# Optimization experiments

Measured on AMD Instinct MI355X. Metric: run time of the kernel, lower is better.

## Reference

```python
import jax, jax.numpy as jnp
import numpy as np

N = 50000      # nodes
E = 800000     # edges (before self loops)
D_IN = 64      # input atom feature dim
HID = 128      # hidden_dim
HEADS = 4
C = HID // HEADS  # 32 per-head channels
ED = 12        # edge feature dim
L = 4          # num GAT layers
EPS = 1e-5


def setup_inputs() -> dict:
    key = jax.random.key(0)
    ks = jax.random.split(key, 10)
    s = 0.1
    return {
        "x": jax.random.normal(ks[0], (N, D_IN), jnp.float32),
        "edge_index": jax.random.randint(ks[1], (2, E), 0, N, dtype=jnp.int32),
        "edge_attr": jax.random.uniform(ks[2], (E, ED), jnp.float32),
        "Wp": jax.random.normal(ks[3], (D_IN, HID), jnp.float32) * s,
        "bp": jnp.zeros((HID,), jnp.float32),
        "W": jax.random.normal(ks[4], (L, HID, HID), jnp.float32) * s,
        "We": jax.random.normal(ks[5], (L, ED, HID), jnp.float32) * s,
        "att_src": jax.random.normal(ks[6], (L, HEADS, C), jnp.float32) * s,
        "att_dst": jax.random.normal(ks[7], (L, HEADS, C), jnp.float32) * s,
        "att_edge": jax.random.normal(ks[8], (L, HEADS, C), jnp.float32) * s,
        "bias": jnp.zeros((L, HID), jnp.float32),
        "gamma": jnp.ones((L, HID), jnp.float32),
        "beta": jnp.zeros((L, HID), jnp.float32),
    }


def _gat_layer(h, src, dst, ea_full, W, We, a_s, a_d, a_e, b):
    # PyG GATConv: x' = x W -> [N, heads, C]; attention uses edge features, msg = alpha * x'_src
    xp = (h @ W).reshape(N, HEADS, C)
    e_emb = (ea_full @ We).reshape(-1, HEADS, C)          # [E', heads, C]
    a_src = (xp * a_s).sum(-1)                            # [N, heads]
    a_dst = (xp * a_d).sum(-1)
    a = a_src[src] + a_dst[dst] + (e_emb * a_e).sum(-1)   # [E', heads]
    a = jax.nn.leaky_relu(a, 0.2)
    # segment softmax over destination node neighborhoods
    amax = jax.ops.segment_max(a, dst, num_segments=N)
    ex = jnp.exp(a - amax[dst])
    denom = jax.ops.segment_sum(ex, dst, num_segments=N)
    alpha = ex / denom[dst]                               # [E', heads]
    msg = alpha[:, :, None] * xp[src]                     # [E', heads, C]
    out = jax.ops.segment_sum(msg, dst, num_segments=N)   # [N, heads, C]
    return out.reshape(N, HID) + b


def reference(x, edge_index, edge_attr, Wp, bp, W, We, att_src, att_dst, att_edge, bias, gamma, beta):
    # PyG GATConv add_self_loops=True with fill_value='mean' for edge_attr
    loop = jnp.arange(N, dtype=edge_index.dtype)
    src = jnp.concatenate([edge_index[0], loop])
    dst = jnp.concatenate([edge_index[1], loop])
    ea_mean = edge_attr.mean(0)
    ea_full = jnp.concatenate([edge_attr, jnp.broadcast_to(ea_mean, (N, ED))], 0)

    h = jax.nn.relu(x @ Wp + bp)
    for i in range(L):
        h_in = h
        h = _gat_layer(h, src, dst, ea_full, W[i], We[i], att_src[i], att_dst[i], att_edge[i], bias[i])
        # BatchNorm1d (training-mode batch statistics)
        mu = h.mean(0)
        var = ((h - mu) ** 2).mean(0)
        h = gamma[i] * (h - mu) / jnp.sqrt(var + EPS) + beta[i]
        h = jax.nn.relu(h)
        if i > 0:
            h = h + h_in
    return h
```

## Files before the change

kernel.cpp:

```cpp
#include <hip/hip_runtime.h>

constexpr int N_NODES = 50000;
constexpr int N_EDGES = 800000;
constexpr int N_ETOT  = N_EDGES + N_NODES;
constexpr int HID     = 128;
constexpr int HEADS   = 4;
constexpr int ED      = 12;
constexpr int LAYERS  = 4;
constexpr float BN_EPS = 1e-5f;
constexpr int EB = (N_ETOT + 255) / 256;
constexpr int GB = (N_NODES + 63) / 64;
constexpr int WB = (LAYERS * HID * HID + 255) / 256;
constexpr int CHUNK  = 2048;
constexpr int NCHUNK = (N_ETOT + CHUNK - 1) / CHUNK;
constexpr int NB     = (N_NODES + 127) / 128;
constexpr int F_TOT  = NB * NCHUNK;
constexpr int SB3    = (F_TOT + 255) / 256;

typedef __attribute__((ext_vector_type(8))) short short8;
typedef __attribute__((ext_vector_type(4))) float floatx4;

__device__ inline unsigned bf16pair(float a, float b) {
    unsigned ua = __float_as_uint(a), ub = __float_as_uint(b);
    ua = (ua + 0x7FFFu + ((ua >> 16) & 1u)) >> 16;
    ub = (ub + 0x7FFFu + ((ub >> 16) & 1u)) >> 16;
    return ua | (ub << 16);
}

__launch_bounds__(256)
__global__ void pre1_kernel(const int* __restrict__ dst, int* __restrict__ counts,
                            const float* __restrict__ ea, float* __restrict__ easum,
                            const float* __restrict__ W, unsigned short* __restrict__ wb,
                            const float* __restrict__ A, const float* __restrict__ B,
                            const float* __restrict__ bias, float* __restrict__ C,
                            unsigned* __restrict__ Cb) {
    __shared__ float smem[64 * 128];
    int bid = blockIdx.x, t = threadIdx.x;
    if (bid < GB) {
        constexpr int K = 64;
        const float4* B4 = (const float4*)B;
        float4* Bs4 = (float4*)smem;
#pragma unroll
        for (int i = t; i < K * 32; i += 256) Bs4[i] = B4[i];
        __syncthreads();

        int c0 = (t & 15) * 8;
        int r0 = (t >> 4) * 4;
        int rbase = bid * 64 + r0;

        float acc[4][8];
#pragma unroll
        for (int j = 0; j < 4; j++)
#pragma unroll
            for (int c = 0; c < 8; c++) acc[j][c] = 0.f;

        const float4* A4 = (const float4*)A;
        int rg[4];
#pragma unroll
        for (int j = 0; j < 4; j++) rg[j] = min(rbase + j, N_NODES - 1);

        for (int kk = 0; kk < K; kk += 4) {
            float4 av[4];
#pragma unroll
            for (int j = 0; j < 4; j++) av[j] = A4[(size_t)rg[j] * (K / 4) + (kk >> 2)];
            float a_arr[4][4];
#pragma unroll
            for (int j = 0; j < 4; j++) {
                a_arr[j][0] = av[j].x; a_arr[j][1] = av[j].y;
                a_arr[j][2] = av[j].z; a_arr[j][3] = av[j].w;
            }
#pragma unroll
            for (int jj = 0; jj < 4; jj++) {
                float4 b0 = Bs4[(kk + jj) * 32 + (c0 >> 2)];
                float4 b1 = Bs4[(kk + jj) * 32 + (c0 >> 2) + 1];
#pragma unroll
                for (int j = 0; j < 4; j++) {
                    float a = a_arr[j][jj];
                    acc[j][0] += a * b0.x; acc[j][1] += a * b0.y;
                    acc[j][2] += a * b0.z; acc[j][3] += a * b0.w;
                    acc[j][4] += a * b1.x; acc[j][5] += a * b1.y;
                    acc[j][6] += a * b1.z; acc[j][7] += a * b1.w;
                }
            }
        }

#pragma unroll
        for (int j = 0; j < 4; j++) {
            int r = rbase + j;
            if (r < N_NODES) {
                float o[8];
#pragma unroll
                for (int c = 0; c < 8; c++) o[c] = fmaxf(acc[j][c] + bias[c0 + c], 0.f);
                ((float4*)(C + (size_t)r * 128 + c0))[0] = make_float4(o[0], o[1], o[2], o[3]);
                ((float4*)(C + (size_t)r * 128 + c0 + 4))[0] = make_float4(o[4], o[5], o[6], o[7]);
                uint4 pk;
                pk.x = bf16pair(o[0], o[1]); pk.y = bf16pair(o[2], o[3]);
                pk.z = bf16pair(o[4], o[5]); pk.w = bf16pair(o[6], o[7]);
                ((uint4*)(Cb + (size_t)r * 64 + (c0 >> 1)))[0] = pk;
            }
        }
    } else if (bid < GB + NCHUNK) {
        int chunk = bid - GB;
        int* lh = (int*)smem;
        for (int i = t; i < NB; i += 256) lh[i] = 0;
        __syncthreads();
        int e0 = chunk * CHUNK;
        int eend = min(e0 + CHUNK, N_ETOT);
        for (int e = e0 + t; e < eend; e += 256) {
            int d = (e < N_EDGES) ? dst[e] : (e - N_EDGES);
            atomicAdd(&lh[d >> 7], 1);
        }
        __syncthreads();
        for (int i = t; i < NB; i += 256) counts[(size_t)chunk * NB + i] = lh[i];
    } else if (bid < GB + NCHUNK + 256) {
        int b2 = bid - GB - NCHUNK;
        float* ls = smem;
        if (t < 12) ls[t] = 0.f;
        __syncthreads();
        float loc[12];
#pragma unroll
        for (int d = 0; d < 12; d++) loc[d] = 0.f;
        for (int e = b2 * 256 + t; e < N_EDGES; e += 256 * 256) {
            const float* er = ea + (size_t)e * ED;
#pragma unroll
            for (int d = 0; d < 12; d++) loc[d] += er[d];
        }
#pragma unroll
        for (int d = 0; d < 12; d++) atomicAdd(&ls[d], loc[d]);
        __syncthreads();
        if (t < 12) atomicAdd(&easum[t], ls[t]);
    } else {
        int idx = (bid - GB - NCHUNK - 256) * 256 + t;
        if (idx < LAYERS * HID * HID) {
            int l = idx >> 14;
            int k = (idx >> 7) & 127;
            int n = idx & 127;
            unsigned u = __float_as_uint(W[idx]);
            u = (u + 0x7FFFu + ((u >> 16) & 1u)) >> 16;
            int kt = k >> 5, q = (k & 31) >> 3, j = k & 7;
            int nt = n >> 4, c = n & 15;
            int lane = q * 16 + c;
            wb[(size_t)l * 16384 + ((size_t)(kt * 8 + nt) * 64 + lane) * 8 + j] =
                (unsigned short)u;
        }
    }
}

__global__ void blocksum2_kernel(const int* __restrict__ counts, int* __restrict__ bsum) {
    __shared__ int sd[256];
    int t = threadIdx.x;
    int j = blockIdx.x * 256 + t;
    int v = 0;
    if (j < F_TOT) {
        int bb = j / NCHUNK, cc = j - bb * NCHUNK;
        v = counts[(size_t)cc * NB + bb];
    }
    sd[t] = v;
    __syncthreads();
#pragma unroll
    for (int off = 128; off; off >>= 1) {
        if (t < off) sd[t] += sd[t + off];
        __syncthreads();
    }
    if (t == 0) bsum[blockIdx.x] = sd[0];
}

__launch_bounds__(256)
__global__ void pre2_kernel(const int* __restrict__ bsum, int* __restrict__ boff,
                            int* __restrict__ chunkbase, int* __restrict__ rowp,
                            const float* __restrict__ easum,
                            const float* __restrict__ We, const float* __restrict__ att_edge,
                            float* __restrict__ wea_all, float* __restrict__ aloop) {
    int t = threadIdx.x;
    if (blockIdx.x == 0) {
        __shared__ int sd[256];
        int b = 3 * t;
        int v0 = (b + 0 < SB3) ? bsum[b + 0] : 0;
        int v1 = (b + 1 < SB3) ? bsum[b + 1] : 0;
        int v2 = (b + 2 < SB3) ? bsum[b + 2] : 0;
        int tot = v0 + v1 + v2;
        sd[t] = tot;
        __syncthreads();
#pragma unroll
        for (int off = 1; off < 256; off <<= 1) {
            int u = (t >= off) ? sd[t - off] : 0;
            __syncthreads();
            sd[t] += u;
            __syncthreads();
        }
        int excl = sd[t] - tot;
        if (b + 0 < SB3) boff[b + 0] = excl;
        if (b + 1 < SB3) boff[b + 1] = excl + v0;
        if (b + 2 < SB3) boff[b + 2] = excl + v0 + v1;
        if (t == 255) {
            chunkbase[F_TOT] = sd[255];
            rowp[N_NODES] = N_ETOT;
        }
    } else {
        __shared__ float em[12];
        __shared__ float weash[LAYERS * ED * HEADS];
        if (t < 12) em[t] = easum[t] / (float)N_EDGES;
        if (t < LAYERS * ED * HEADS) {
            int l = t / (ED * HEADS);
            int r = t % (ED * HEADS);
            int d = r / HEADS;
            int h = r % HEADS;
            float sum = 0.f;
#pragma unroll
            for (int c = 0; c < 32; c++)
                sum += We[((size_t)(l * ED + d)) * HID + h * 32 + c] *
                       att_edge[(l * HEADS + h) * 32 + c];
            wea_all[t] = sum;
            weash[t] = sum;
        }
        __syncthreads();
        if (t < LAYERS * HEADS) {
            int l = t / HEADS, h = t % HEADS;
            float s = 0.f;
#pragma unroll
            for (int d = 0; d < 12; d++) s += em[d] * weash[l * ED * HEADS + d * HEADS + h];
            aloop[t] = s;
        }
    }
}

__global__ void addback_kernel(const int* __restrict__ counts, const int* __restrict__ boff,
                               int* __restrict__ chunkbase) {
    __shared__ int sd[256];
    int t = threadIdx.x;
    int j = blockIdx.x * 256 + t;
    int v = 0;
    if (j < F_TOT) {
        int bb = j / NCHUNK, cc = j - bb * NCHUNK;
        v = counts[(size_t)cc * NB + bb];
    }
    sd[t] = v;
    __syncthreads();
#pragma unroll
    for (int off = 1; off < 256; off <<= 1) {
        int u = (t >= off) ? sd[t - off] : 0;
        __syncthreads();
        sd[t] += u;
        __syncthreads();
    }
    if (j < F_TOT) chunkbase[j] = sd[t] - v + boff[blockIdx.x];
}

__launch_bounds__(256)
__global__ void pre3_kernel(const unsigned short* __restrict__ hAb,
                            const unsigned short* __restrict__ wb,
                            const float* __restrict__ att_s, const float* __restrict__ att_d,
                            unsigned* __restrict__ xpb,
                            float* __restrict__ asrc, float* __restrict__ adst,
                            const int* __restrict__ src, const int* __restrict__ dst,
                            const int* __restrict__ chunkbase, int2* __restrict__ bucketed) {
    __shared__ float smem[4 * 16 * 129];
    int t = threadIdx.x;
    if (blockIdx.x >= GB) {
        int chunk = blockIdx.x - GB;
        int* lb = (int*)smem;
        int* lh = lb + NB;
        for (int i = t; i < NB; i += 256) {
            lb[i] = chunkbase[(size_t)i * NCHUNK + chunk];
            lh[i] = 0;
        }
        __syncthreads();
        int e0 = chunk * CHUNK;
        int eend = min(e0 + CHUNK, N_ETOT);
        for (int e = e0 + t; e < eend; e += 256) {
            int s, d;
            if (e < N_EDGES) { s = src[e]; d = dst[e]; }
            else             { s = d = e - N_EDGES; }
            int b = d >> 7;
            int lr = atomicAdd(&lh[b], 1);
            bucketed[lb[b] + lr] = make_int2(s, e | ((d & 127) << 20));
        }
        return;
    }
    int bid = blockIdx.x;
    float (*lds)[16][129] = (float (*)[16][129])smem;
    int w = t >> 6, lane = t & 63;
    int rbase = bid * 64 + w * 16;
    int mrow = lane & 15, quad = lane >> 4;

    floatx4 acc[8];
#pragma unroll
    for (int nt = 0; nt < 8; nt++) acc[nt] = (floatx4){0.f, 0.f, 0.f, 0.f};

    int arow = min(rbase + mrow, N_NODES - 1);
    const short8* wb8 = (const short8*)wb;
#pragma unroll
    for (int kt = 0; kt < 4; kt++) {
        short8 afrag = *(const short8*)(hAb + (size_t)arow * 128 + kt * 32 + quad * 8);
#pragma unroll
        for (int nt = 0; nt < 8; nt++) {
            short8 bfrag = wb8[(kt * 8 + nt) * 64 + lane];
            acc[nt] = __builtin_amdgcn_mfma_f32_16x16x32_bf16(afrag, bfrag, acc[nt], 0, 0, 0);
        }
    }
#pragma unroll
    for (int nt = 0; nt < 8; nt++)
#pragma unroll
        for (int rr = 0; rr < 4; rr++)
            lds[w][quad * 4 + rr][nt * 16 + mrow] = acc[nt][rr];

    int row = lane >> 2, h = lane & 3;
    int r = rbase + row;
    float vals[32];
    float ps = 0.f, pd = 0.f;
#pragma unroll
    for (int c = 0; c < 32; c++) {
        float v = lds[w][row][h * 32 + c];
        vals[c] = v;
        ps += v * att_s[h * 32 + c];
        pd += v * att_d[h * 32 + c];
    }
    if (r < N_NODES) {
        unsigned* dstp = xpb + (size_t)r * 64 + h * 16;
#pragma unroll
        for (int qq = 0; qq < 4; qq++) {
            uint4 o;
            o.x = bf16pair(vals[qq * 8 + 0], vals[qq * 8 + 1]);
            o.y = bf16pair(vals[qq * 8 + 2], vals[qq * 8 + 3]);
            o.z = bf16pair(vals[qq * 8 + 4], vals[qq * 8 + 5]);
            o.w = bf16pair(vals[qq * 8 + 6], vals[qq * 8 + 7]);
            ((uint4*)dstp)[qq] = o;
        }
        asrc[r * 4 + h] = ps;
        adst[r * 4 + h] = pd;
    }
}

__launch_bounds__(256)
__global__ void csrd_kernel(const int2* __restrict__ bucketed, const int* __restrict__ chunkbase,
                            int2* __restrict__ csr, int* __restrict__ rowp) {
    __shared__ int hist[128], exc[128], cur[128];
    int b = blockIdx.x, t = threadIdx.x;
    int base = chunkbase[(size_t)b * NCHUNK];
    int cend = chunkbase[(size_t)(b + 1) * NCHUNK];
    int cnt = cend - base;
    if (t < 128) { hist[t] = 0; cur[t] = 0; }
    __syncthreads();
    for (int i = t; i < cnt; i += 256)
        atomicAdd(&hist[(bucketed[base + i].y >> 20) & 127], 1);
    __syncthreads();
    if (t < 128) exc[t] = hist[t];
    __syncthreads();
#pragma unroll
    for (int off = 1; off < 128; off <<= 1) {
        int u = (t < 128 && t >= off) ? exc[t - off] : 0;
        __syncthreads();
        if (t < 128) exc[t] += u;
        __syncthreads();
    }
    if (t < 128) {
        exc[t] -= hist[t];
        int node = b * 128 + t;
        if (node < N_NODES) rowp[node] = base + exc[t];
    }
    __syncthreads();
    for (int i = t; i < cnt; i += 256) {
        int2 r = bucketed[base + i];
        int dl = (r.y >> 20) & 127;
        int lr = atomicAdd(&cur[dl], 1);
        csr[base + exc[dl] + lr] = make_int2(r.x, r.y & 0xFFFFF);
    }
}

__launch_bounds__(256)
__global__ void pre4_kernel(const int2* __restrict__ csr, const float* __restrict__ ea,
                            const float* __restrict__ wea_all, const float* __restrict__ aloop,
                            uint2* __restrict__ aecsr) {
    __shared__ float wsh[LAYERS * ED * HEADS];
    __shared__ float lsh[LAYERS * HEADS];
    int t = threadIdx.x;
    if (t < LAYERS * ED * HEADS) wsh[t] = wea_all[t];
    if (t < LAYERS * HEADS) lsh[t] = aloop[t];
    __syncthreads();
    int i = blockIdx.x * 256 + t;
    if (i >= N_ETOT) return;
    int e = csr[i].y;
    float a[LAYERS][4];
    if (e < N_EDGES) {
        float er[12];
        const float* ep = ea + (size_t)e * ED;
#pragma unroll
        for (int d = 0; d < 12; d++) er[d] = ep[d];
#pragma unroll
        for (int l = 0; l < LAYERS; l++)
#pragma unroll
            for (int h = 0; h < 4; h++) {
                float s = 0.f;
#pragma unroll
                for (int d = 0; d < 12; d++) s += er[d] * wsh[l * 48 + d * 4 + h];
                a[l][h] = s;
            }
    } else {
#pragma unroll
        for (int l = 0; l < LAYERS; l++)
#pragma unroll
            for (int h = 0; h < 4; h++) a[l][h] = lsh[l * 4 + h];
    }
#pragma unroll
    for (int l = 0; l < LAYERS; l++)
        aecsr[(size_t)l * N_ETOT + i] =
            make_uint2(bf16pair(a[l][0], a[l][1]), bf16pair(a[l][2], a[l][3]));
}

template <int ADD>
__launch_bounds__(256)
__global__ void gemm_fused_kernel(const float* __restrict__ outb,
                                  const float* __restrict__ bnsum,
                                  const float* __restrict__ bnsum2,
                                  const float* __restrict__ gamma,
                                  const float* __restrict__ beta,
                                  float* __restrict__ hA,
                                  const unsigned short* __restrict__ wb,
                                  const float* __restrict__ att_s,
                                  const float* __restrict__ att_d,
                                  unsigned* __restrict__ xpb,
                                  float* __restrict__ asrc, float* __restrict__ adst) {
    __shared__ float lds[4][16][129];
    __shared__ float sc_s[128], sh_s[128];
    int t = threadIdx.x;
    if (t < 128) {
        float mu = bnsum[t] / (float)N_NODES;
        float var = bnsum2[t] / (float)N_NODES - mu * mu;
        float inv = rsqrtf(var + BN_EPS);
        float g = gamma[t] * inv;
        sc_s[t] = g;
        sh_s[t] = beta[t] - mu * g;
    }
    __syncthreads();

    int w = t >> 6, lane = t & 63;
    int rbase = blockIdx.x * 64 + w * 16;
    int mrow = lane & 15, quad = lane >> 4;
    int arow = rbase + mrow;
    bool owner = arow < N_NODES;
    int ar = min(arow, N_NODES - 1);

    floatx4 acc[8];
#pragma unroll
    for (int nt = 0; nt < 8; nt++) acc[nt] = (floatx4){0.f, 0.f, 0.f, 0.f};

    const short8* wb8 = (const short8*)wb;
#pragma unroll
    for (int kt = 0; kt < 4; kt++) {
        int cb = kt * 32 + quad * 8;
        const float4* ob = (const float4*)(outb + (size_t)ar * 128 + cb);
        float4 o0 = ob[0], o1 = ob[1];
        float v[8];
        v[0] = fmaxf(o0.x * sc_s[cb + 0] + sh_s[cb + 0], 0.f);
        v[1] = fmaxf(o0.y * sc_s[cb + 1] + sh_s[cb + 1], 0.f);
        v[2] = fmaxf(o0.z * sc_s[cb + 2] + sh_s[cb + 2], 0.f);
        v[3] = fmaxf(o0.w * sc_s[cb + 3] + sh_s[cb + 3], 0.f);
        v[4] = fmaxf(o1.x * sc_s[cb + 4] + sh_s[cb + 4], 0.f);
        v[5] = fmaxf(o1.y * sc_s[cb + 5] + sh_s[cb + 5], 0.f);
        v[6] = fmaxf(o1.z * sc_s[cb + 6] + sh_s[cb + 6], 0.f);
        v[7] = fmaxf(o1.w * sc_s[cb + 7] + sh_s[cb + 7], 0.f);
        if (ADD) {
            const float4* hp = (const float4*)(hA + (size_t)ar * 128 + cb);
            float4 h0 = hp[0], h1 = hp[1];
            v[0] += h0.x; v[1] += h0.y; v[2] += h0.z; v[3] += h0.w;
            v[4] += h1.x; v[5] += h1.y; v[6] += h1.z; v[7] += h1.w;
        }
        if (owner) {
            float4* hw = (float4*)(hA + (size_t)ar * 128 + cb);
            hw[0] = make_float4(v[0], v[1], v[2], v[3]);
            hw[1] = make_float4(v[4], v[5], v[6], v[7]);
        }
        uint4 pk;
        pk.x = bf16pair(v[0], v[1]); pk.y = bf16pair(v[2], v[3]);
        pk.z = bf16pair(v[4], v[5]); pk.w = bf16pair(v[6], v[7]);
        short8 afrag = *(short8*)&pk;
#pragma unroll
        for (int nt = 0; nt < 8; nt++) {
            short8 bfrag = wb8[(kt * 8 + nt) * 64 + lane];
            acc[nt] = __builtin_amdgcn_mfma_f32_16x16x32_bf16(afrag, bfrag, acc[nt], 0, 0, 0);
        }
    }

#pragma unroll
    for (int nt = 0; nt < 8; nt++)
#pragma unroll
        for (int rr = 0; rr < 4; rr++)
            lds[w][quad * 4 + rr][nt * 16 + mrow] = acc[nt][rr];

    int row = lane >> 2, h = lane & 3;
    int r = rbase + row;
    float vals[32];
    float ps = 0.f, pd = 0.f;
#pragma unroll
    for (int c = 0; c < 32; c++) {
        float v = lds[w][row][h * 32 + c];
        vals[c] = v;
        ps += v * att_s[h * 32 + c];
        pd += v * att_d[h * 32 + c];
    }
    if (r < N_NODES) {
        unsigned* dstp = xpb + (size_t)r * 64 + h * 16;
#pragma unroll
        for (int qq = 0; qq < 4; qq++) {
            uint4 o;
            o.x = bf16pair(vals[qq * 8 + 0], vals[qq * 8 + 1]);
            o.y = bf16pair(vals[qq * 8 + 2], vals[qq * 8 + 3]);
            o.z = bf16pair(vals[qq * 8 + 4], vals[qq * 8 + 5]);
            o.w = bf16pair(vals[qq * 8 + 6], vals[qq * 8 + 7]);
            ((uint4*)dstp)[qq] = o;
        }
        asrc[r * 4 + h] = ps;
        adst[r * 4 + h] = pd;
    }
}

__launch_bounds__(256)
__global__ void node_kernel(const uint2* __restrict__ aecsr, const float* __restrict__ asrc,
                            const float* __restrict__ adst, const int* __restrict__ rowp,
                            const int2* __restrict__ csr, const unsigned* __restrict__ xpb,
                            float* __restrict__ out) {
    int gw = (blockIdx.x * blockDim.x + threadIdx.x) >> 6;
    int lane = threadIdx.x & 63;
    if (gw >= N_NODES) return;
    int sub = lane >> 3;
    int sl  = lane & 7;
    int h   = sl >> 1;
    int beg = rowp[gw], end = rowp[gw + 1];
    const uint4* xp4 = (const uint4*)xpb;
    float adh = adst[gw * 4 + h];

    float a[16];
#pragma unroll
    for (int c = 0; c < 16; c++) a[c] = 0.f;
    float den = 0.f;

#define PROC(JJ)                                                                 \
    {                                                                            \
        int2 se = csr[JJ];                                                       \
        uint2 ae = aecsr[JJ];                                                    \
        unsigned aw = (h & 2) ? ae.y : ae.x;                                     \
        float aeh = __uint_as_float((h & 1) ? (aw & 0xFFFF0000u) : (aw << 16));  \
        float ash = asrc[se.x * 4 + h];                                          \
        uint4 v0 = xp4[(size_t)se.x * 16 + sl * 2];                              \
        uint4 v1 = xp4[(size_t)se.x * 16 + sl * 2 + 1];                          \
        float lg = ash + adh + aeh;                                              \
        lg = (lg > 0.f) ? lg : 0.2f * lg;                                        \
        float ex = __expf(fminf(lg, 60.f));                                      \
        a[0]  += ex * __uint_as_float(v0.x << 16);                               \
        a[1]  += ex * __uint_as_float(v0.x & 0xFFFF0000u);                       \
        a[2]  += ex * __uint_as_float(v0.y << 16);                               \
        a[3]  += ex * __uint_as_float(v0.y & 0xFFFF0000u);                       \
        a[4]  += ex * __uint_as_float(v0.z << 16);                               \
        a[5]  += ex * __uint_as_float(v0.z & 0xFFFF0000u);                       \
        a[6]  += ex * __uint_as_float(v0.w << 16);                               \
        a[7]  += ex * __uint_as_float(v0.w & 0xFFFF0000u);                       \
        a[8]  += ex * __uint_as_float(v1.x << 16);                               \
        a[9]  += ex * __uint_as_float(v1.x & 0xFFFF0000u);                       \
        a[10] += ex * __uint_as_float(v1.y << 16);                               \
        a[11] += ex * __uint_as_float(v1.y & 0xFFFF0000u);                       \
        a[12] += ex * __uint_as_float(v1.z << 16);                               \
        a[13] += ex * __uint_as_float(v1.z & 0xFFFF0000u);                       \
        a[14] += ex * __uint_as_float(v1.w << 16);                               \
        a[15] += ex * __uint_as_float(v1.w & 0xFFFF0000u);                       \
        den += ex;                                                               \
    }

    int j = beg + sub;
    for (; j + 8 < end; j += 16) {
        PROC(j); PROC(j + 8);
    }
    for (; j < end; j += 8) PROC(j);
#undef PROC

#pragma unroll
    for (int c = 0; c < 16; c++) {
        a[c] += __shfl_xor(a[c], 8);
        a[c] += __shfl_xor(a[c], 16);
        a[c] += __shfl_xor(a[c], 32);
    }
    den += __shfl_xor(den, 8);
    den += __shfl_xor(den, 16);
    den += __shfl_xor(den, 32);
    float inv = 1.0f / den;
    if (sub == 0) {
        float* op = out + (size_t)gw * 128 + sl * 16;
        ((float4*)op)[0] = make_float4(a[0] * inv, a[1] * inv, a[2] * inv, a[3] * inv);
        ((float4*)op)[1] = make_float4(a[4] * inv, a[5] * inv, a[6] * inv, a[7] * inv);
        ((float4*)op)[2] = make_float4(a[8] * inv, a[9] * inv, a[10] * inv, a[11] * inv);
        ((float4*)op)[3] = make_float4(a[12] * inv, a[13] * inv, a[14] * inv, a[15] * inv);
    }
}

__launch_bounds__(256)
__global__ void bnstats_kernel(const float* __restrict__ h, float* __restrict__ bnsum,
                               float* __restrict__ bnsum2) {
    __shared__ float ls[256], ls2[256];
    int t = threadIdx.x;
    int c = t & 127, half = t >> 7;
    int r0 = blockIdx.x * 128;
    float s = 0.f, s2 = 0.f;
    int rend = min(r0 + 128, N_NODES);
    for (int r = r0 + half; r < rend; r += 2) {
        float v = h[(size_t)r * 128 + c];
        s += v; s2 += v * v;
    }
    ls[t] = s; ls2[t] = s2;
    __syncthreads();
    if (half == 0) {
        s += ls[t + 128]; s2 += ls2[t + 128];
        atomicAdd(&bnsum[c], s);
        atomicAdd(&bnsum2[c], s2);
    }
}

__launch_bounds__(256)
__global__ void finalupd_kernel(const float* __restrict__ outb, const float* __restrict__ bnsum,
                                const float* __restrict__ bnsum2, const float* __restrict__ gamma,
                                const float* __restrict__ beta, const float* __restrict__ hA,
                                float* __restrict__ dst) {
    __shared__ float sc_s[128], sh_s[128];
    int t = threadIdx.x;
    if (t < 128) {
        float mu = bnsum[t] / (float)N_NODES;
        float var = bnsum2[t] / (float)N_NODES - mu * mu;
        float inv = rsqrtf(var + BN_EPS);
        float g = gamma[t] * inv;
        sc_s[t] = g;
        sh_s[t] = beta[t] - mu * g;
    }
    __syncthreads();
    int i = blockIdx.x * blockDim.x + t;
    if (i >= N_NODES * 32) return;
    int c4 = (i & 31) * 4;
    float4 o = ((const float4*)outb)[i];
    float4 hh = ((const float4*)hA)[i];
    float4 v;
    v.x = fmaxf(o.x * sc_s[c4 + 0] + sh_s[c4 + 0], 0.f) + hh.x;
    v.y = fmaxf(o.y * sc_s[c4 + 1] + sh_s[c4 + 1], 0.f) + hh.y;
    v.z = fmaxf(o.z * sc_s[c4 + 2] + sh_s[c4 + 2], 0.f) + hh.z;
    v.w = fmaxf(o.w * sc_s[c4 + 3] + sh_s[c4 + 3], 0.f) + hh.w;
    ((float4*)dst)[i] = v;
}

extern "C" void kernel_launch(void* const* d_in, const int* in_sizes, int n_in,
                              void* d_out, int out_size, void* d_ws, size_t ws_size,
                              hipStream_t stream) {
    const float* x          = (const float*)d_in[0];
    const int*   edge_index = (const int*)d_in[1];
    const float* edge_attr  = (const float*)d_in[2];
    const float* Wp         = (const float*)d_in[3];
    const float* bp         = (const float*)d_in[4];
    const float* W          = (const float*)d_in[5];
    const float* We         = (const float*)d_in[6];
    const float* att_src    = (const float*)d_in[7];
    const float* att_dst    = (const float*)d_in[8];
    const float* att_edge   = (const float*)d_in[9];
    const float* gamma      = (const float*)d_in[11];
    const float* beta       = (const float*)d_in[12];
    float* outp = (float*)d_out;

    const int* ei_src = edge_index;
    const int* ei_dst = edge_index + N_EDGES;

    char* p = (char*)d_ws;
    auto alloc = [&](size_t nbytes) {
        char* r = p;
        p += (nbytes + 255) & ~(size_t)255;
        return r;
    };
    float* easum    = (float*)alloc(16 * 4);
    float* bnsumall = (float*)alloc((size_t)LAYERS * 256 * 4);
    size_t zero_bytes = (char*)(bnsumall + LAYERS * 256) - (char*)easum;

    float* hA       = (float*)alloc((size_t)N_NODES * 128 * 4);
    unsigned* hAb   = (unsigned*)alloc((size_t)N_NODES * 64 * 4);
    unsigned* xpb   = (unsigned*)alloc((size_t)N_NODES * 64 * 4);
    float* outb     = (float*)alloc((size_t)N_NODES * 128 * 4);
    float* asrc     = (float*)alloc((size_t)N_NODES * 4 * 4);
    float* adst     = (float*)alloc((size_t)N_NODES * 4 * 4);
    float* wea_all  = (float*)alloc((LAYERS * 48 + 16) * 4);
    float* aloop    = wea_all + LAYERS * 48;
    unsigned short* wb = (unsigned short*)alloc((size_t)LAYERS * 16384 * 2);
    int* rowp       = (int*)alloc(((size_t)N_NODES + 1) * 4);
    int* counts     = (int*)alloc((size_t)F_TOT * 4);
    int* chunkbase  = (int*)alloc(((size_t)F_TOT + 1) * 4);
    int2* bucketed  = (int2*)alloc((size_t)N_ETOT * 8);
    int2* csr       = (int2*)alloc((size_t)N_ETOT * 8);
    uint2* aecsr    = (uint2*)alloc((size_t)LAYERS * N_ETOT * 8);
    int* bsum       = (int*)alloc(1024 * 4);
    int* boff       = (int*)alloc(1024 * 4);

    (void)hipMemsetAsync(easum, 0, zero_bytes, stream);

    pre1_kernel<<<GB + NCHUNK + 256 + WB, 256, 0, stream>>>(
        ei_dst, counts, edge_attr, easum, W, wb, x, Wp, bp, hA, hAb);
    blocksum2_kernel<<<SB3, 256, 0, stream>>>(counts, bsum);
    pre2_kernel<<<2, 256, 0, stream>>>(bsum, boff, chunkbase, rowp, easum, We, att_edge,
                                       wea_all, aloop);
    addback_kernel<<<SB3, 256, 0, stream>>>(counts, boff, chunkbase);
    pre3_kernel<<<GB + NCHUNK, 256, 0, stream>>>(
        (const unsigned short*)hAb, wb, att_src, att_dst, xpb, asrc, adst,
        ei_src, ei_dst, chunkbase, bucketed);
    csrd_kernel<<<NB, 256, 0, stream>>>(bucketed, chunkbase, csr, rowp);
    pre4_kernel<<<EB, 256, 0, stream>>>(csr, edge_attr, wea_all, aloop, aecsr);

    for (int l = 0; l < LAYERS; l++) {
        float* bnsum  = bnsumall + l * 256;
        float* bnsum2 = bnsum + 128;
        node_kernel<<<(N_NODES + 3) / 4, 256, 0, stream>>>(
            aecsr + (size_t)l * N_ETOT, asrc, adst, rowp, csr, xpb, outb);
        bnstats_kernel<<<(N_NODES + 127) / 128, 256, 0, stream>>>(outb, bnsum, bnsum2);
        if (l < LAYERS - 1) {
            if (l == 0)
                gemm_fused_kernel<0><<<GB, 256, 0, stream>>>(
                    outb, bnsum, bnsum2, gamma + l * 128, beta + l * 128, hA,
                    wb + (size_t)(l + 1) * 16384, att_src + (l + 1) * 128,
                    att_dst + (l + 1) * 128, xpb, asrc, adst);
            else
                gemm_fused_kernel<1><<<GB, 256, 0, stream>>>(
                    outb, bnsum, bnsum2, gamma + l * 128, beta + l * 128, hA,
                    wb + (size_t)(l + 1) * 16384, att_src + (l + 1) * 128,
                    att_dst + (l + 1) * 128, xpb, asrc, adst);
        } else {
            finalupd_kernel<<<(N_NODES * 32 + 255) / 256, 256, 0, stream>>>(
                outb, bnsum, bnsum2, gamma + l * 128, beta + l * 128, hA, outp);
        }
    }
}
```

Before: 575.2 us.

## Fuse BatchNorm statistics into node aggregation kernel and prefetch GEMM A rows

The separate bnstats pass that re-read the full aggregated output is removed. Each node_kernel block now writes per-block channel sums and sums of squares, built through shared memory, to a partial buffer, and a small bnred kernel reduces these with atomics. The GEMM A-tile loads are also software-prefetched one k-step ahead. This saves a full read of the N×128 output per layer, at the cost of a __syncthreads in node_kernel and an extra partial buffer of NODE_BLKS×256 floats. The early return for out-of-range warps was removed, but N_NODES is divisible by 4, so every warp is valid.

```diff
diff --git a/kernel.cpp b/kernel.cpp
--- a/kernel.cpp
+++ b/kernel.cpp
@@ -11,6 +11,7 @@
 constexpr int EB = (N_ETOT + 255) / 256;
 constexpr int GB = (N_NODES + 63) / 64;
 constexpr int WB = (LAYERS * HID * HID + 255) / 256;
+constexpr int NODE_BLKS = (N_NODES + 3) / 4;
 constexpr int CHUNK  = 2048;
 constexpr int NCHUNK = (N_ETOT + CHUNK - 1) / CHUNK;
 constexpr int NB     = (N_NODES + 127) / 128;
@@ -59,10 +60,16 @@
 #pragma unroll
         for (int j = 0; j < 4; j++) rg[j] = min(rbase + j, N_NODES - 1);
 
+        float4 av[4];
+#pragma unroll
+        for (int j = 0; j < 4; j++) av[j] = A4[(size_t)rg[j] * (K / 4)];
+
         for (int kk = 0; kk < K; kk += 4) {
-            float4 av[4];
-#pragma unroll
-            for (int j = 0; j < 4; j++) av[j] = A4[(size_t)rg[j] * (K / 4) + (kk >> 2)];
+            int kn = (kk + 4 < K) ? ((kk + 4) >> 2) : (kk >> 2);
+            float4 avn[4];
+#pragma unroll
+            for (int j = 0; j < 4; j++) avn[j] = A4[(size_t)rg[j] * (K / 4) + kn];
+
             float a_arr[4][4];
 #pragma unroll
             for (int j = 0; j < 4; j++) {
@@ -82,6 +89,8 @@
                     acc[j][6] += a * b1.z; acc[j][7] += a * b1.w;
                 }
             }
+#pragma unroll
+            for (int j = 0; j < 4; j++) av[j] = avn[j];
         }
 
 #pragma unroll
@@ -518,10 +527,11 @@
 __global__ void node_kernel(const uint2* __restrict__ aecsr, const float* __restrict__ asrc,
                             const float* __restrict__ adst, const int* __restrict__ rowp,
                             const int2* __restrict__ csr, const unsigned* __restrict__ xpb,
-                            float* __restrict__ out) {
+                            float* __restrict__ out, float* __restrict__ partial) {
+    __shared__ float ps[4][256];
     int gw = (blockIdx.x * blockDim.x + threadIdx.x) >> 6;
     int lane = threadIdx.x & 63;
-    if (gw >= N_NODES) return;
+    int wib = threadIdx.x >> 6;
     int sub = lane >> 3;
     int sl  = lane & 7;
     int h   = sl >> 1;
@@ -583,34 +593,34 @@
     den += __shfl_xor(den, 32);
     float inv = 1.0f / den;
     if (sub == 0) {
+        float vv[16];
+#pragma unroll
+        for (int c = 0; c < 16; c++) vv[c] = a[c] * inv;
         float* op = out + (size_t)gw * 128 + sl * 16;
-        ((float4*)op)[0] = make_float4(a[0] * inv, a[1] * inv, a[2] * inv, a[3] * inv);
-        ((float4*)op)[1] = make_float4(a[4] * inv, a[5] * inv, a[6] * inv, a[7] * inv);
-        ((float4*)op)[2] = make_float4(a[8] * inv, a[9] * inv, a[10] * inv, a[11] * inv);
-        ((float4*)op)[3] = make_float4(a[12] * inv, a[13] * inv, a[14] * inv, a[15] * inv);
-    }
-}
-
-__launch_bounds__(256)
-__global__ void bnstats_kernel(const float* __restrict__ h, float* __restrict__ bnsum,
-                               float* __restrict__ bnsum2) {
-    __shared__ float ls[256], ls2[256];
+        ((float4*)op)[0] = make_float4(vv[0], vv[1], vv[2], vv[3]);
+        ((float4*)op)[1] = make_float4(vv[4], vv[5], vv[6], vv[7]);
+        ((float4*)op)[2] = make_float4(vv[8], vv[9], vv[10], vv[11]);
+        ((float4*)op)[3] = make_float4(vv[12], vv[13], vv[14], vv[15]);
+#pragma unroll
+        for (int c = 0; c < 16; c++) {
+            int ch = sl * 16 + c;
+            ps[wib][ch] = vv[c];
+            ps[wib][128 + ch] = vv[c] * vv[c];
+        }
+    }
+    __syncthreads();
+    int t2 = threadIdx.x;
+    float s = ps[0][t2] + ps[1][t2] + ps[2][t2] + ps[3][t2];
+    partial[(size_t)blockIdx.x * 256 + t2] = s;
+}
+
+__launch_bounds__(256)
+__global__ void bnred_kernel(const float* __restrict__ partial, float* __restrict__ bn) {
     int t = threadIdx.x;
-    int c = t & 127, half = t >> 7;
-    int r0 = blockIdx.x * 128;
-    float s = 0.f, s2 = 0.f;
-    int rend = min(r0 + 128, N_NODES);
-    for (int r = r0 + half; r < rend; r += 2) {
-        float v = h[(size_t)r * 128 + c];
-        s += v; s2 += v * v;
-    }
-    ls[t] = s; ls2[t] = s2;
-    __syncthreads();
-    if (half == 0) {
-        s += ls[t + 128]; s2 += ls2[t + 128];
-        atomicAdd(&bnsum[c], s);
-        atomicAdd(&bnsum2[c], s2);
-    }
+    float acc = 0.f;
+    for (int r = blockIdx.x; r < NODE_BLKS; r += gridDim.x)
+        acc += partial[(size_t)r * 256 + t];
+    atomicAdd(&bn[t], acc);
 }
 
 __launch_bounds__(256)
@@ -687,6 +697,7 @@
     int2* bucketed  = (int2*)alloc((size_t)N_ETOT * 8);
     int2* csr       = (int2*)alloc((size_t)N_ETOT * 8);
     uint2* aecsr    = (uint2*)alloc((size_t)LAYERS * N_ETOT * 8);
+    float* partial  = (float*)alloc((size_t)NODE_BLKS * 256 * 4);
     int* bsum       = (int*)alloc(1024 * 4);
     int* boff       = (int*)alloc(1024 * 4);
 
@@ -707,9 +718,9 @@
     for (int l = 0; l < LAYERS; l++) {
         float* bnsum  = bnsumall + l * 256;
         float* bnsum2 = bnsum + 128;
-        node_kernel<<<(N_NODES + 3) / 4, 256, 0, stream>>>(
-            aecsr + (size_t)l * N_ETOT, asrc, adst, rowp, csr, xpb, outb);
-        bnstats_kernel<<<(N_NODES + 127) / 128, 256, 0, stream>>>(outb, bnsum, bnsum2);
+        node_kernel<<<NODE_BLKS, 256, 0, stream>>>(
+            aecsr + (size_t)l * N_ETOT, asrc, adst, rowp, csr, xpb, outb, partial);
+        bnred_kernel<<<128, 256, 0, stream>>>(partial, bnsum);
         if (l < LAYERS - 1) {
             if (l == 0)
                 gemm_fused_kernel<0><<<GB, 256, 0, stream>>>(
```

Result: slower. 609.6 us (+6.0%).
